# Kernel tuning notes

Measured on AMD Instinct MI355X. Metric: run time of the kernel, lower is better.

The kernel has to match this reference:

```python
import jax, jax.numpy as jnp
import numpy as np

ATOM_FDIM = 35
BOND_FDIM = 5
MAX_NB = 15
HIDDEN = 512
DEPTH = 6
N_MOLS = 1024
ATOMS_PER_MOL = 32
N_ATOMS = N_MOLS * ATOMS_PER_MOL      # 32768
N_BONDS = 2 * N_ATOMS                  # 65536 (each bond appears in both directions)
N_MESS = 8192                          # tree messages (row 0 is the zero pad slot)
TOTAL_MSG = N_MESS + N_BONDS           # index space for agraph/bgraph


def setup_inputs() -> dict:
    key = jax.random.key(0)
    ks = jax.random.split(key, 8)
    fatoms = jax.random.normal(ks[0], (N_ATOMS, ATOM_FDIM), jnp.float32)
    fbonds = jax.random.normal(ks[1], (N_BONDS, ATOM_FDIM + BOND_FDIM), jnp.float32)
    agraph = jax.random.randint(ks[2], (N_ATOMS, MAX_NB), 0, TOTAL_MSG, dtype=jnp.int32)
    bgraph = jax.random.randint(ks[3], (N_BONDS, MAX_NB), 0, TOTAL_MSG, dtype=jnp.int32)
    # row 0 of the concatenated message table is the padding slot -> zero it
    tree_message = jax.random.normal(ks[4], (N_MESS, HIDDEN), jnp.float32).at[0].set(0.0)
    starts = jnp.arange(N_MOLS, dtype=jnp.int32) * ATOMS_PER_MOL
    scope = jnp.stack([starts, jnp.full((N_MOLS,), ATOMS_PER_MOL, jnp.int32)], axis=1)
    s_i = 1.0 / np.sqrt(ATOM_FDIM + BOND_FDIM)
    s_h = 1.0 / np.sqrt(HIDDEN)
    s_o = 1.0 / np.sqrt(ATOM_FDIM + HIDDEN)
    W_i = jax.random.normal(ks[5], (ATOM_FDIM + BOND_FDIM, HIDDEN), jnp.float32) * s_i
    W_h = jax.random.normal(ks[6], (HIDDEN, HIDDEN), jnp.float32) * s_h
    W_o = jax.random.normal(ks[7], (ATOM_FDIM + HIDDEN, HIDDEN), jnp.float32) * s_o
    b_o = jnp.zeros((HIDDEN,), jnp.float32)
    return {"fatoms": fatoms, "fbonds": fbonds, "agraph": agraph, "bgraph": bgraph,
            "scope": scope, "tree_message": tree_message,
            "W_i": W_i, "W_h": W_h, "W_o": W_o, "b_o": b_o}


def reference(fatoms, fbonds, agraph, bgraph, scope, tree_message, W_i, W_h, W_o, b_o):
    binput = fbonds @ W_i                         # [B, H]
    graph_message = jax.nn.relu(binput)

    def step(gm, _):
        message = jnp.concatenate([tree_message, gm], axis=0)   # [M+B, H]
        nei = message[bgraph].sum(axis=1)                       # gather-sum [B, H]
        return jax.nn.relu(binput + nei @ W_h), None

    graph_message, _ = jax.lax.scan(step, graph_message, None, length=DEPTH - 1)

    message = jnp.concatenate([tree_message, graph_message], axis=0)
    nei = message[agraph].sum(axis=1)             # [A, H]
    ainput = jnp.concatenate([fatoms, nei], axis=1)
    atom_hiddens = jax.nn.relu(ainput @ W_o + b_o)

    # scope is uniform (st = i*ATOMS_PER_MOL, le = ATOMS_PER_MOL) -> static segment ids
    seg = jnp.repeat(jnp.arange(N_MOLS), ATOMS_PER_MOL)
    sums = jax.ops.segment_sum(atom_hiddens, seg, num_segments=N_MOLS)
    return sums / scope[:, 1:].astype(atom_hiddens.dtype)
```

## Files before the change

### kernel.cpp

```cpp
#include <hip/hip_runtime.h>
#include <stdint.h>


#define MAX_NB 15
#define HID 512
#define NMOLS 1024
#define NA 32768
#define NB 65536
#define NMESS 8192

typedef unsigned short u16;
typedef unsigned int u32;
typedef __bf16 bf16x8 __attribute__((ext_vector_type(8)));
typedef float f32x4 __attribute__((ext_vector_type(4)));

__device__ __forceinline__ u16 f2bf(float f) {
  u32 u = __builtin_bit_cast(u32, f);
  u32 r = (u + 0x7fffu + ((u >> 16) & 1u)) >> 16;
  return (u16)r;
}
__device__ __forceinline__ float bf2f(u16 b) {
  u32 u = ((u32)b) << 16;
  return __builtin_bit_cast(float, u);
}

__device__ __forceinline__ void async16(const u16* g, u16* l) {
  __builtin_amdgcn_global_load_lds(
      (const __attribute__((address_space(1))) u32*)g,
      (__attribute__((address_space(3))) u32*)l, 16, 0, 0);
}

__global__ __launch_bounds__(256) void prep_kernel(
    const float* __restrict__ fbonds, const float* __restrict__ tree,
    const float* __restrict__ Wi, const float* __restrict__ Wh,
    const float* __restrict__ Wo,
    u16* __restrict__ msg, u16* __restrict__ fbpad, u16* __restrict__ wi_t,
    u16* __restrict__ wh_t, u16* __restrict__ wo_t) {
  int t = blockIdx.x * 256 + threadIdx.x;
  const int N0 = NMESS * HID;
  const int N1 = NB * 64;
  const int N2 = 512 * 64;
  const int N3 = 512 * 512;
  const int N4 = 512 * 576;
  if (t < N0) { msg[t] = f2bf(tree[t]); return; }
  t -= N0;
  if (t < N1) {
    int row = t >> 6, c = t & 63;
    fbpad[t] = (c < 40) ? f2bf(fbonds[row * 40 + c]) : (u16)0;
    return;
  }
  t -= N1;
  if (t < N2) {
    int n = t >> 6, k = t & 63;
    wi_t[t] = (k < 40) ? f2bf(Wi[k * 512 + n]) : (u16)0;
    return;
  }
  t -= N2;
  if (t < N3) {
    int n = t >> 9, k = t & 511;
    wh_t[t] = f2bf(Wh[k * 512 + n]);
    return;
  }
  t -= N3;
  if (t < N4) {
    int n = t / 576, k = t - n * 576;
    float v = 0.f;
    if (k < 512) v = Wo[(35 + k) * 512 + n];
    else if (k < 547) v = Wo[(k - 512) * 512 + n];
    wo_t[t] = f2bf(v);
    return;
  }
}

__global__ __launch_bounds__(256) void gather_bonds(
    const u16* __restrict__ msg, const int* __restrict__ bgraph,
    u16* __restrict__ nei) {
  int row = blockIdx.x * 4 + (threadIdx.x >> 6);
  int lane = threadIdx.x & 63;
  const int* idx = bgraph + row * MAX_NB;
  float acc[8] = {0, 0, 0, 0, 0, 0, 0, 0};
#pragma unroll
  for (int j = 0; j < MAX_NB; j++) {
    int id = idx[j];
    uint4 v = *(const uint4*)(msg + (size_t)id * HID + lane * 8);
    acc[0] += bf2f((u16)(v.x & 0xffff)); acc[1] += bf2f((u16)(v.x >> 16));
    acc[2] += bf2f((u16)(v.y & 0xffff)); acc[3] += bf2f((u16)(v.y >> 16));
    acc[4] += bf2f((u16)(v.z & 0xffff)); acc[5] += bf2f((u16)(v.z >> 16));
    acc[6] += bf2f((u16)(v.w & 0xffff)); acc[7] += bf2f((u16)(v.w >> 16));
  }
  uint4 o;
  o.x = (u32)f2bf(acc[0]) | ((u32)f2bf(acc[1]) << 16);
  o.y = (u32)f2bf(acc[2]) | ((u32)f2bf(acc[3]) << 16);
  o.z = (u32)f2bf(acc[4]) | ((u32)f2bf(acc[5]) << 16);
  o.w = (u32)f2bf(acc[6]) | ((u32)f2bf(acc[7]) << 16);
  *(uint4*)(nei + (size_t)row * HID + lane * 8) = o;
}

__global__ __launch_bounds__(256) void gather_atoms(
    const u16* __restrict__ msg, const int* __restrict__ agraph,
    const float* __restrict__ fatoms, u16* __restrict__ ainput) {
  int row = blockIdx.x * 4 + (threadIdx.x >> 6);
  int lane = threadIdx.x & 63;
  const int* idx = agraph + row * MAX_NB;
  float acc[8] = {0, 0, 0, 0, 0, 0, 0, 0};
#pragma unroll
  for (int j = 0; j < MAX_NB; j++) {
    int id = idx[j];
    uint4 v = *(const uint4*)(msg + (size_t)id * HID + lane * 8);
    acc[0] += bf2f((u16)(v.x & 0xffff)); acc[1] += bf2f((u16)(v.x >> 16));
    acc[2] += bf2f((u16)(v.y & 0xffff)); acc[3] += bf2f((u16)(v.y >> 16));
    acc[4] += bf2f((u16)(v.z & 0xffff)); acc[5] += bf2f((u16)(v.z >> 16));
    acc[6] += bf2f((u16)(v.w & 0xffff)); acc[7] += bf2f((u16)(v.w >> 16));
  }
  uint4 o;
  o.x = (u32)f2bf(acc[0]) | ((u32)f2bf(acc[1]) << 16);
  o.y = (u32)f2bf(acc[2]) | ((u32)f2bf(acc[3]) << 16);
  o.z = (u32)f2bf(acc[4]) | ((u32)f2bf(acc[5]) << 16);
  o.w = (u32)f2bf(acc[6]) | ((u32)f2bf(acc[7]) << 16);
  u16* arow = ainput + (size_t)row * 576;
  *(uint4*)(arow + lane * 8) = o;
  float tv = (lane < 35) ? fatoms[(size_t)row * 35 + lane] : 0.f;
  arow[512 + lane] = f2bf(tv);
}

template <int EPI>
__global__ __launch_bounds__(256) void gemm_k(
    const u16* __restrict__ A, const u16* __restrict__ Bt, int K,
    u16* __restrict__ binput, u16* __restrict__ msgout,
    const float* __restrict__ bo, const int* __restrict__ scope,
    float* __restrict__ out) {
  __shared__ __align__(16) u16 As[128 * 32];
  __shared__ __align__(16) u16 Bs[128 * 32];
  const int t = threadIdx.x;
  const int lane = t & 63;
  const int w = t >> 6;
  const int wm = w & 1, wn = w >> 1;
  const int mBase = blockIdx.x * 128;
  const int nBase = blockIdx.y * 128;
  const int r = t >> 2;
  const int c8 = (t & 3) * 8;
  const int q8 = (lane >> 4) * 8;
  const int l15 = lane & 15;

  f32x4 acc[4][4];
#pragma unroll
  for (int i = 0; i < 4; i++)
#pragma unroll
    for (int j = 0; j < 4; j++)
#pragma unroll
      for (int rg = 0; rg < 4; rg++) acc[i][j][rg] = 0.f;

  for (int kb = 0; kb < K; kb += 32) {
    __syncthreads();
    async16(A + (size_t)(mBase + r) * K + kb + c8, As + r * 32 + c8);
    async16(A + (size_t)(mBase + r + 64) * K + kb + c8, As + (r + 64) * 32 + c8);
    async16(Bt + (size_t)(nBase + r) * K + kb + c8, Bs + r * 32 + c8);
    async16(Bt + (size_t)(nBase + r + 64) * K + kb + c8, Bs + (r + 64) * 32 + c8);
    __syncthreads();
    bf16x8 av[4], bv[4];
#pragma unroll
    for (int i = 0; i < 4; i++)
      av[i] = *(const bf16x8*)(As + (wm * 64 + i * 16 + l15) * 32 + q8);
#pragma unroll
    for (int j = 0; j < 4; j++)
      bv[j] = *(const bf16x8*)(Bs + (wn * 64 + j * 16 + l15) * 32 + q8);
#pragma unroll
    for (int i = 0; i < 4; i++)
#pragma unroll
      for (int j = 0; j < 4; j++)
        acc[i][j] = __builtin_amdgcn_mfma_f32_16x16x32_bf16(av[i], bv[j],
                                                            acc[i][j], 0, 0, 0);
  }

  if (EPI == 2) {
#pragma unroll
    for (int m = 0; m < 2; m++) {
      int mol = (mBase + wm * 64 + m * 32) >> 5;
      float inv_le = 1.0f / (float)scope[mol * 2 + 1];
#pragma unroll
      for (int j = 0; j < 4; j++) {
        int col = nBase + wn * 64 + j * 16 + l15;
        float bias = bo[col];
        float s = 0.f;
#pragma unroll
        for (int i = 2 * m; i < 2 * m + 2; i++)
#pragma unroll
          for (int rg = 0; rg < 4; rg++)
            s += fmaxf(acc[i][j][rg] + bias, 0.f);
        s += __shfl_xor(s, 16, 64);
        s += __shfl_xor(s, 32, 64);
        if (lane < 16) out[(size_t)mol * HID + col] = s * inv_le;
      }
    }
  } else {
#pragma unroll
    for (int i = 0; i < 4; i++) {
      int row = mBase + wm * 64 + i * 16 + (lane >> 4) * 4;
#pragma unroll
      for (int j = 0; j < 4; j++) {
        int col = nBase + wn * 64 + j * 16 + l15;
#pragma unroll
        for (int rg = 0; rg < 4; rg++) {
          float v = acc[i][j][rg];
          size_t gi = (size_t)(row + rg) * HID + col;
          if (EPI == 0) {
            binput[gi] = f2bf(v);
            msgout[gi + (size_t)NMESS * HID] = f2bf(fmaxf(v, 0.f));
          } else {
            v += bf2f(binput[gi]);
            msgout[gi + (size_t)NMESS * HID] = f2bf(fmaxf(v, 0.f));
          }
        }
      }
    }
  }
}

extern "C" void kernel_launch(void* const* d_in, const int* in_sizes, int n_in,
                              void* d_out, int out_size, void* d_ws,
                              size_t ws_size, hipStream_t stream) {
  const float* fatoms = (const float*)d_in[0];
  const float* fbonds = (const float*)d_in[1];
  const int* agraph = (const int*)d_in[2];
  const int* bgraph = (const int*)d_in[3];
  const int* scope = (const int*)d_in[4];
  const float* tree = (const float*)d_in[5];
  const float* Wi = (const float*)d_in[6];
  const float* Wh = (const float*)d_in[7];
  const float* Wo = (const float*)d_in[8];
  const float* bo = (const float*)d_in[9];
  float* out = (float*)d_out;

  char* ws = (char*)d_ws;
  u16* msg = (u16*)(ws);
  u16* binput = (u16*)(ws + 75497472ull);
  u16* nei = (u16*)(ws + 142606336ull);
  u16* wi_t = (u16*)(ws + 209715200ull);
  u16* wh_t = (u16*)(ws + 209780736ull);
  u16* wo_t = (u16*)(ws + 210305024ull);
  u16* fbpad = nei;
  u16* ainput = binput;

  prep_kernel<<<35072, 256, 0, stream>>>(fbonds, tree, Wi, Wh, Wo, msg, fbpad,
                                         wi_t, wh_t, wo_t);

  dim3 gB(NB / 128, 4);
  gemm_k<0><<<gB, 256, 0, stream>>>(fbpad, wi_t, 64, binput, msg, nullptr,
                                    nullptr, nullptr);
  for (int d = 0; d < 5; d++) {
    gather_bonds<<<NB / 4, 256, 0, stream>>>(msg, bgraph, nei);
    gemm_k<1><<<gB, 256, 0, stream>>>(nei, wh_t, 512, binput, msg, nullptr,
                                      nullptr, nullptr);
  }
  gather_atoms<<<NA / 4, 256, 0, stream>>>(msg, agraph, fatoms, ainput);
  dim3 gO(NA / 128, 4);
  gemm_k<2><<<gO, 256, 0, stream>>>(ainput, wo_t, 576, nullptr, nullptr, bo,
                                    scope, out);
}
```

Baseline: 1.292 ms.

## Fuse neighbor gather-sum into GEMM A-tile load with ping-pong message buffers

Removes the separate gather kernels and the materialized nei/ainput buffers. Each GEMM block now gathers its 64 rows' neighbor sums chunk by chunk straight into LDS and runs MFMA against the full 512-wide N. Two graph-message buffers are alternated, and tree messages are read from their own buffer. B operands are read directly from global memory instead of being staged in LDS, and the gather latency now sits inside the GEMM main loop with no overlap.

Result: slower. 1.335 ms (+3.3%).

```diff
diff --git a/kernel.cpp b/kernel.cpp
--- a/kernel.cpp
+++ b/kernel.cpp
@@ -4,7 +4,6 @@
 
 #define MAX_NB 15
 #define HID 512
-#define NMOLS 1024
 #define NA 32768
 #define NB 65536
 #define NMESS 8192
@@ -23,6 +22,12 @@
   u32 u = ((u32)b) << 16;
   return __builtin_bit_cast(float, u);
 }
+__device__ __forceinline__ float bflo(u32 u) {
+  return __builtin_bit_cast(float, u << 16);
+}
+__device__ __forceinline__ float bfhi(u32 u) {
+  return __builtin_bit_cast(float, u & 0xffff0000u);
+}
 
 __device__ __forceinline__ void async16(const u16* g, u16* l) {
   __builtin_amdgcn_global_load_lds(
@@ -33,16 +38,16 @@
 __global__ __launch_bounds__(256) void prep_kernel(
     const float* __restrict__ fbonds, const float* __restrict__ tree,
     const float* __restrict__ Wi, const float* __restrict__ Wh,
-    const float* __restrict__ Wo,
-    u16* __restrict__ msg, u16* __restrict__ fbpad, u16* __restrict__ wi_t,
-    u16* __restrict__ wh_t, u16* __restrict__ wo_t) {
+    const float* __restrict__ Wo, u16* __restrict__ tree_bf,
+    u16* __restrict__ fbpad, u16* __restrict__ wi_t, u16* __restrict__ wh_t,
+    u16* __restrict__ wo_t) {
   int t = blockIdx.x * 256 + threadIdx.x;
   const int N0 = NMESS * HID;
   const int N1 = NB * 64;
   const int N2 = 512 * 64;
   const int N3 = 512 * 512;
   const int N4 = 512 * 576;
-  if (t < N0) { msg[t] = f2bf(tree[t]); return; }
+  if (t < N0) { tree_bf[t] = f2bf(tree[t]); return; }
   t -= N0;
   if (t < N1) {
     int row = t >> 6, c = t & 63;
@@ -72,63 +77,10 @@
   }
 }
 
-__global__ __launch_bounds__(256) void gather_bonds(
-    const u16* __restrict__ msg, const int* __restrict__ bgraph,
-    u16* __restrict__ nei) {
-  int row = blockIdx.x * 4 + (threadIdx.x >> 6);
-  int lane = threadIdx.x & 63;
-  const int* idx = bgraph + row * MAX_NB;
-  float acc[8] = {0, 0, 0, 0, 0, 0, 0, 0};
-#pragma unroll
-  for (int j = 0; j < MAX_NB; j++) {
-    int id = idx[j];
-    uint4 v = *(const uint4*)(msg + (size_t)id * HID + lane * 8);
-    acc[0] += bf2f((u16)(v.x & 0xffff)); acc[1] += bf2f((u16)(v.x >> 16));
-    acc[2] += bf2f((u16)(v.y & 0xffff)); acc[3] += bf2f((u16)(v.y >> 16));
-    acc[4] += bf2f((u16)(v.z & 0xffff)); acc[5] += bf2f((u16)(v.z >> 16));
-    acc[6] += bf2f((u16)(v.w & 0xffff)); acc[7] += bf2f((u16)(v.w >> 16));
-  }
-  uint4 o;
-  o.x = (u32)f2bf(acc[0]) | ((u32)f2bf(acc[1]) << 16);
-  o.y = (u32)f2bf(acc[2]) | ((u32)f2bf(acc[3]) << 16);
-  o.z = (u32)f2bf(acc[4]) | ((u32)f2bf(acc[5]) << 16);
-  o.w = (u32)f2bf(acc[6]) | ((u32)f2bf(acc[7]) << 16);
-  *(uint4*)(nei + (size_t)row * HID + lane * 8) = o;
-}
-
-__global__ __launch_bounds__(256) void gather_atoms(
-    const u16* __restrict__ msg, const int* __restrict__ agraph,
-    const float* __restrict__ fatoms, u16* __restrict__ ainput) {
-  int row = blockIdx.x * 4 + (threadIdx.x >> 6);
-  int lane = threadIdx.x & 63;
-  const int* idx = agraph + row * MAX_NB;
-  float acc[8] = {0, 0, 0, 0, 0, 0, 0, 0};
-#pragma unroll
-  for (int j = 0; j < MAX_NB; j++) {
-    int id = idx[j];
-    uint4 v = *(const uint4*)(msg + (size_t)id * HID + lane * 8);
-    acc[0] += bf2f((u16)(v.x & 0xffff)); acc[1] += bf2f((u16)(v.x >> 16));
-    acc[2] += bf2f((u16)(v.y & 0xffff)); acc[3] += bf2f((u16)(v.y >> 16));
-    acc[4] += bf2f((u16)(v.z & 0xffff)); acc[5] += bf2f((u16)(v.z >> 16));
-    acc[6] += bf2f((u16)(v.w & 0xffff)); acc[7] += bf2f((u16)(v.w >> 16));
-  }
-  uint4 o;
-  o.x = (u32)f2bf(acc[0]) | ((u32)f2bf(acc[1]) << 16);
-  o.y = (u32)f2bf(acc[2]) | ((u32)f2bf(acc[3]) << 16);
-  o.z = (u32)f2bf(acc[4]) | ((u32)f2bf(acc[5]) << 16);
-  o.w = (u32)f2bf(acc[6]) | ((u32)f2bf(acc[7]) << 16);
-  u16* arow = ainput + (size_t)row * 576;
-  *(uint4*)(arow + lane * 8) = o;
-  float tv = (lane < 35) ? fatoms[(size_t)row * 35 + lane] : 0.f;
-  arow[512 + lane] = f2bf(tv);
-}
-
-template <int EPI>
-__global__ __launch_bounds__(256) void gemm_k(
-    const u16* __restrict__ A, const u16* __restrict__ Bt, int K,
-    u16* __restrict__ binput, u16* __restrict__ msgout,
-    const float* __restrict__ bo, const int* __restrict__ scope,
-    float* __restrict__ out) {
+__global__ __launch_bounds__(256) void init_gemm(
+    const u16* __restrict__ A, const u16* __restrict__ Bt,
+    u16* __restrict__ binput, u16* __restrict__ gm0) {
+  const int K = 64;
   __shared__ __align__(16) u16 As[128 * 32];
   __shared__ __align__(16) u16 Bs[128 * 32];
   const int t = threadIdx.x;
@@ -171,15 +123,109 @@
         acc[i][j] = __builtin_amdgcn_mfma_f32_16x16x32_bf16(av[i], bv[j],
                                                             acc[i][j], 0, 0, 0);
   }
-
-  if (EPI == 2) {
+#pragma unroll
+  for (int i = 0; i < 4; i++) {
+    int row = mBase + wm * 64 + i * 16 + (lane >> 4) * 4;
+#pragma unroll
+    for (int j = 0; j < 4; j++) {
+      int col = nBase + wn * 64 + j * 16 + l15;
+#pragma unroll
+      for (int rg = 0; rg < 4; rg++) {
+        float v = acc[i][j][rg];
+        size_t gi = (size_t)(row + rg) * HID + col;
+        binput[gi] = f2bf(v);
+        gm0[gi] = f2bf(fmaxf(v, 0.f));
+      }
+    }
+  }
+}
+
+template <int OUT>
+__global__ __launch_bounds__(512, 4) void fused_step(
+    const u16* __restrict__ tree, const u16* __restrict__ gm_prev,
+    const int* __restrict__ graph, const u16* __restrict__ Bt,
+    const u16* __restrict__ binput, u16* __restrict__ gm_next,
+    const float* __restrict__ fatoms, const float* __restrict__ bo,
+    const int* __restrict__ scope, float* __restrict__ out) {
+  const int K = OUT ? 576 : 512;
+  const int NCH = K / 64;
+  __shared__ __align__(16) u16 As[64 * 72];
+  const int t = threadIdx.x;
+  const int lane = t & 63;
+  const int w = t >> 6;
+  const int l15 = lane & 15;
+  const int q8 = (lane >> 4) * 8;
+  const int mBase = blockIdx.x * 64;
+  const int slot = t >> 3;
+  const int sub = t & 7;
+
+  f32x4 acc[4][4];
+#pragma unroll
+  for (int i = 0; i < 4; i++)
+#pragma unroll
+    for (int j = 0; j < 4; j++)
+#pragma unroll
+      for (int rg = 0; rg < 4; rg++) acc[i][j][rg] = 0.f;
+
+  const int* idx = graph + (size_t)(mBase + slot) * MAX_NB;
+  const u16* gm_sh = gm_prev - (size_t)NMESS * HID;
+
+  for (int ch = 0; ch < NCH; ch++) {
+    const int kb = ch * 64;
+    __syncthreads();
+    float g[8] = {0.f, 0.f, 0.f, 0.f, 0.f, 0.f, 0.f, 0.f};
+    if (OUT && ch == NCH - 1) {
+#pragma unroll
+      for (int e = 0; e < 8; e++) {
+        int c = sub * 8 + e;
+        g[e] = (c < 35) ? fatoms[(size_t)(mBase + slot) * 35 + c] : 0.f;
+      }
+    } else {
+#pragma unroll
+      for (int j = 0; j < MAX_NB; j++) {
+        int id = idx[j];
+        const u16* base = (id < NMESS) ? tree : gm_sh;
+        uint4 v = *(const uint4*)(base + (size_t)id * HID + kb + sub * 8);
+        g[0] += bflo(v.x); g[1] += bfhi(v.x);
+        g[2] += bflo(v.y); g[3] += bfhi(v.y);
+        g[4] += bflo(v.z); g[5] += bfhi(v.z);
+        g[6] += bflo(v.w); g[7] += bfhi(v.w);
+      }
+    }
+    uint4 o;
+    o.x = (u32)f2bf(g[0]) | ((u32)f2bf(g[1]) << 16);
+    o.y = (u32)f2bf(g[2]) | ((u32)f2bf(g[3]) << 16);
+    o.z = (u32)f2bf(g[4]) | ((u32)f2bf(g[5]) << 16);
+    o.w = (u32)f2bf(g[6]) | ((u32)f2bf(g[7]) << 16);
+    *(uint4*)(As + slot * 72 + sub * 8) = o;
+    __syncthreads();
+#pragma unroll
+    for (int s = 0; s < 2; s++) {
+      bf16x8 av[4], bv[4];
+#pragma unroll
+      for (int i = 0; i < 4; i++)
+        av[i] = *(const bf16x8*)(As + (i * 16 + l15) * 72 + s * 32 + q8);
+#pragma unroll
+      for (int j = 0; j < 4; j++)
+        bv[j] = *(const bf16x8*)(Bt + (size_t)(w * 64 + j * 16 + l15) * K + kb +
+                                 s * 32 + q8);
+#pragma unroll
+      for (int i = 0; i < 4; i++)
+#pragma unroll
+        for (int j = 0; j < 4; j++)
+          acc[i][j] = __builtin_amdgcn_mfma_f32_16x16x32_bf16(
+              av[i], bv[j], acc[i][j], 0, 0, 0);
+    }
+  }
+
+  if (OUT) {
 #pragma unroll
     for (int m = 0; m < 2; m++) {
-      int mol = (mBase + wm * 64 + m * 32) >> 5;
+      int mol = (mBase >> 5) + m;
       float inv_le = 1.0f / (float)scope[mol * 2 + 1];
 #pragma unroll
       for (int j = 0; j < 4; j++) {
-        int col = nBase + wn * 64 + j * 16 + l15;
+        int col = w * 64 + j * 16 + l15;
         float bias = bo[col];
         float s = 0.f;
 #pragma unroll
@@ -195,21 +241,15 @@
   } else {
 #pragma unroll
     for (int i = 0; i < 4; i++) {
-      int row = mBase + wm * 64 + i * 16 + (lane >> 4) * 4;
+      int row = mBase + i * 16 + (lane >> 4) * 4;
 #pragma unroll
       for (int j = 0; j < 4; j++) {
-        int col = nBase + wn * 64 + j * 16 + l15;
+        int col = w * 64 + j * 16 + l15;
 #pragma unroll
         for (int rg = 0; rg < 4; rg++) {
-          float v = acc[i][j][rg];
           size_t gi = (size_t)(row + rg) * HID + col;
-          if (EPI == 0) {
-            binput[gi] = f2bf(v);
-            msgout[gi + (size_t)NMESS * HID] = f2bf(fmaxf(v, 0.f));
-          } else {
-            v += bf2f(binput[gi]);
-            msgout[gi + (size_t)NMESS * HID] = f2bf(fmaxf(v, 0.f));
-          }
+          float v = acc[i][j][rg] + bf2f(binput[gi]);
+          gm_next[gi] = f2bf(fmaxf(v, 0.f));
         }
       }
     }
@@ -232,28 +272,30 @@
   float* out = (float*)d_out;
 
   char* ws = (char*)d_ws;
-  u16* msg = (u16*)(ws);
-  u16* binput = (u16*)(ws + 75497472ull);
-  u16* nei = (u16*)(ws + 142606336ull);
+  u16* tree_bf = (u16*)(ws);
+  u16* gmA = (u16*)(ws + 8388608ull);
+  u16* gmB = (u16*)(ws + 75497472ull);
+  u16* binput = (u16*)(ws + 142606336ull);
   u16* wi_t = (u16*)(ws + 209715200ull);
   u16* wh_t = (u16*)(ws + 209780736ull);
   u16* wo_t = (u16*)(ws + 210305024ull);
-  u16* fbpad = nei;
-  u16* ainput = binput;
-
-  prep_kernel<<<35072, 256, 0, stream>>>(fbonds, tree, Wi, Wh, Wo, msg, fbpad,
-                                         wi_t, wh_t, wo_t);
-
-  dim3 gB(NB / 128, 4);
-  gemm_k<0><<<gB, 256, 0, stream>>>(fbpad, wi_t, 64, binput, msg, nullptr,
-                                    nullptr, nullptr);
+  u16* fbpad = gmB;
+
+  prep_kernel<<<35072, 256, 0, stream>>>(fbonds, tree, Wi, Wh, Wo, tree_bf,
+                                         fbpad, wi_t, wh_t, wo_t);
+
+  init_gemm<<<dim3(NB / 128, 4), 256, 0, stream>>>(fbpad, wi_t, binput, gmA);
+
+  u16* prev = gmA;
+  u16* next = gmB;
   for (int d = 0; d < 5; d++) {
-    gather_bonds<<<NB / 4, 256, 0, stream>>>(msg, bgraph, nei);
-    gemm_k<1><<<gB, 256, 0, stream>>>(nei, wh_t, 512, binput, msg, nullptr,
-                                      nullptr, nullptr);
-  }
-  gather_atoms<<<NA / 4, 256, 0, stream>>>(msg, agraph, fatoms, ainput);
-  dim3 gO(NA / 128, 4);
-  gemm_k<2><<<gO, 256, 0, stream>>>(ainput, wo_t, 576, nullptr, nullptr, bo,
-                                    scope, out);
-}
+    fused_step<0><<<NB / 64, 512, 0, stream>>>(tree_bf, prev, bgraph, wh_t,
+                                               binput, next, nullptr, nullptr,
+                                               nullptr, nullptr);
+    u16* tmp = prev; prev = next; next = tmp;
+  }
+
+  fused_step<1><<<NA / 64, 512, 0, stream>>>(tree_bf, prev, agraph, wo_t,
+                                             nullptr, nullptr, fatoms, bo,
+                                             scope, out);
+}
```
